# Optimization experiments

Hardware: AMD Instinct MI355X
Metric: run time of the kernel (lower is better)

The kernel has to match this reference:

```python
import jax, jax.numpy as jnp
import numpy as np

N, LQ, C, M, L, P = 8, 2048, 256, 8, 4, 4
DH = C // M  # 32
LENS = (2048, 1024, 512, 256)


def setup_inputs() -> dict:
    key = jax.random.key(0)
    ks = jax.random.split(key, 8)
    s = 1.0 / np.sqrt(C)
    return {
        "query": jax.random.normal(ks[0], (N, LQ, C), jnp.float32),
        "reference_points": jax.random.uniform(ks[1], (N, LQ, L, 1), jnp.float32),
        "input_flatten": jax.random.normal(ks[2], (N, sum(LENS), C), jnp.float32),
        "temporal_lens": np.array(LENS, np.int64),
        "level_start_index": np.array([0, 2048, 3072, 3584], np.int64),
        "W_off": jax.random.normal(ks[3], (C, M * L * P), jnp.float32) * 0.01,
        "b_off": jax.random.normal(ks[4], (M * L * P,), jnp.float32),
        "W_attn": jax.random.normal(ks[5], (C, M * L * P), jnp.float32) * 0.01,
        "b_attn": jnp.zeros((M * L * P,), jnp.float32),
        "W_val": jax.random.normal(ks[6], (C, C), jnp.float32) * s,
        "b_val": jnp.zeros((C,), jnp.float32),
        "W_out": jax.random.normal(ks[7], (C, C), jnp.float32) * s,
        "b_out": jnp.zeros((C,), jnp.float32),
    }


def _deform_core(value, lens, loc, attn):
    # value: (N, S, M, DH); loc, attn: (N, LQ, M, L, P); loc in normalized [0,1] coords.
    # Equivalent to per-level F.grid_sample (bilinear, zeros padding, align_corners=False)
    # on a 1xT image: pixel position = loc*T - 0.5; the y-coord 0.5 lands exactly on row 0.
    outs = []
    start = 0
    for l, T in enumerate(lens):
        v = value[:, start:start + T].transpose(0, 2, 1, 3)  # (N, M, T, DH)
        start += T
        pos = loc[..., l, :] * T - 0.5                       # (N, LQ, M, P)
        x0f = jnp.floor(pos)
        frac = pos - x0f
        x0 = x0f.astype(jnp.int32)

        def gather(idx):
            i = jnp.clip(idx, 0, T - 1).transpose(0, 2, 1, 3).reshape(N, M, LQ * P, 1)
            return jnp.take_along_axis(v, i, axis=2).reshape(N, M, LQ, P, DH)

        in0 = ((x0 >= 0) & (x0 < T)).astype(value.dtype)
        in1 = ((x0 + 1 >= 0) & (x0 + 1 < T)).astype(value.dtype)
        w0 = ((1.0 - frac) * in0).transpose(0, 2, 1, 3)[..., None]  # (N, M, LQ, P, 1)
        w1 = (frac * in1).transpose(0, 2, 1, 3)[..., None]
        outs.append(gather(x0) * w0 + gather(x0 + 1) * w1)          # (N, M, LQ, P, DH)
    sampled = jnp.stack(outs, axis=3)          # (N, M, LQ, L, P, DH)
    aw = attn.transpose(0, 2, 1, 3, 4)         # (N, M, LQ, L, P)
    return jnp.einsum('nmqlpd,nmqlp->nqmd', sampled, aw).reshape(N, LQ, C)


def reference(query, reference_points, input_flatten, temporal_lens, level_start_index,
              W_off, b_off, W_attn, b_attn, W_val, b_val, W_out, b_out):
    lens = [int(t) for t in np.asarray(temporal_lens)[:L]]  # static per-level lengths
    value = (input_flatten @ W_val + b_val).reshape(N, -1, M, DH)
    off = (query @ W_off + b_off).reshape(N, LQ, M, L, P)
    attn = jax.nn.softmax((query @ W_attn + b_attn).reshape(N, LQ, M, L * P), axis=-1)
    attn = attn.reshape(N, LQ, M, L, P)
    norm = jnp.asarray(lens, query.dtype)                    # offset_normalizer (L,)
    loc = reference_points[:, :, None, :, None, 0] + off / norm[None, None, None, :, None]
    out = _deform_core(value, lens, loc, attn)
    out = out @ W_out + b_out
    return out, loc, attn
```

## Files before the change

### kernel.cpp

```cpp
#include <hip/hip_runtime.h>
#include <hip/hip_bf16.h>
#include <math.h>

#define NB 8
#define LQ 2048
#define CCH 256
#define MH 8
#define SSUM 3840

typedef unsigned short ushort_t;
typedef unsigned int uint_t;
typedef __attribute__((ext_vector_type(8))) short bf16x8;
typedef __attribute__((ext_vector_type(4))) float f32x4;

__device__ inline ushort_t f2bf(float f) {
  __hip_bfloat16 h = __float2bfloat16(f);
  return *reinterpret_cast<ushort_t*>(&h);
}
__device__ inline float bf2f_lo(uint_t u) {
  union { uint_t u32; float f; } x;
  x.u32 = u << 16;
  return x.f;
}
__device__ inline float bf2f_hi(uint_t u) {
  union { uint_t u32; float f; } x;
  x.u32 = u & 0xffff0000u;
  return x.f;
}

__global__ __launch_bounds__(256) void prep_all(
    const float* __restrict__ Wv, const float* __restrict__ Wo,
    const float* __restrict__ Woff, const float* __restrict__ Wattn,
    ushort_t* __restrict__ BtVal, ushort_t* __restrict__ BtOut,
    ushort_t* __restrict__ BtOA) {
  int b = blockIdx.x;
  int k = threadIdx.x;
  if (b < 256) {
    BtVal[b * 256 + k] = f2bf(Wv[(size_t)k * 256 + b]);
  } else if (b < 512) {
    int n = b - 256;
    BtOut[n * 256 + k] = f2bf(Wo[(size_t)k * 256 + n]);
  } else if (b < 640) {
    int n = b - 512;
    BtOA[n * 256 + k] = f2bf(Woff[(size_t)k * 128 + n]);
  } else {
    int n = b - 640;
    BtOA[(128 + n) * 256 + k] = f2bf(Wattn[(size_t)k * 128 + n]);
  }
}

template <typename AT, typename OT>
__global__ __launch_bounds__(256) void gemm_mfma(
    const AT* __restrict__ A, const ushort_t* __restrict__ Bt,
    const float* __restrict__ bias0, const float* __restrict__ bias1,
    OT* __restrict__ C0, OT* __restrict__ C1,
    int Nsplit, int Cstride) {
  __shared__ ushort_t Abf[2][128][24];
  __shared__ ushort_t Bbf[2][128][24];

  const int tid = threadIdx.x;
  const int bm = blockIdx.y * 128;
  const int bn = blockIdx.x * 128;

  const int lane = tid & 63;
  const int wv = tid >> 6;
  const int wm = (wv >> 1) * 64;
  const int wn = (wv & 1) * 64;
  const int quad = lane >> 4;
  const int l16 = lane & 15;

  const int sr = tid & 127;
  const int sh = tid >> 7;

  f32x4 acc[4][4];
#pragma unroll
  for (int i = 0; i < 4; ++i)
#pragma unroll
    for (int j = 0; j < 4; ++j) acc[i][j] = (f32x4)(0.f);

  for (int k0 = 0; k0 < 256; k0 += 32) {
    uint4 aq0, aq1;
    if constexpr (sizeof(AT) == 4) {
      const float* gp = (const float*)A + (size_t)(bm + sr) * 256 + k0 + sh * 16;
      float4 f0 = *(const float4*)(gp + 0);
      float4 f1 = *(const float4*)(gp + 4);
      float4 f2 = *(const float4*)(gp + 8);
      float4 f3 = *(const float4*)(gp + 12);
      aq0.x = (uint_t)f2bf(f0.x) | ((uint_t)f2bf(f0.y) << 16);
      aq0.y = (uint_t)f2bf(f0.z) | ((uint_t)f2bf(f0.w) << 16);
      aq0.z = (uint_t)f2bf(f1.x) | ((uint_t)f2bf(f1.y) << 16);
      aq0.w = (uint_t)f2bf(f1.z) | ((uint_t)f2bf(f1.w) << 16);
      aq1.x = (uint_t)f2bf(f2.x) | ((uint_t)f2bf(f2.y) << 16);
      aq1.y = (uint_t)f2bf(f2.z) | ((uint_t)f2bf(f2.w) << 16);
      aq1.z = (uint_t)f2bf(f3.x) | ((uint_t)f2bf(f3.y) << 16);
      aq1.w = (uint_t)f2bf(f3.z) | ((uint_t)f2bf(f3.w) << 16);
    } else {
      const ushort_t* gp = (const ushort_t*)A + (size_t)(bm + sr) * 256 + k0 + sh * 16;
      aq0 = *(const uint4*)(gp + 0);
      aq1 = *(const uint4*)(gp + 8);
    }
    const ushort_t* gb = Bt + (size_t)(bn + sr) * 256 + k0 + sh * 16;
    uint4 bq0 = *(const uint4*)(gb + 0);
    uint4 bq1 = *(const uint4*)(gb + 8);

    __syncthreads();
    *(uint4*)&Abf[sh][sr][0] = aq0;
    *(uint4*)&Abf[sh][sr][8] = aq1;
    *(uint4*)&Bbf[sh][sr][0] = bq0;
    *(uint4*)&Bbf[sh][sr][8] = bq1;
    __syncthreads();

    bf16x8 af[4], bfr[4];
#pragma unroll
    for (int mi = 0; mi < 4; ++mi)
      af[mi] = *(const bf16x8*)&Abf[quad >> 1][wm + mi * 16 + l16][(quad & 1) * 8];
#pragma unroll
    for (int ni = 0; ni < 4; ++ni)
      bfr[ni] = *(const bf16x8*)&Bbf[quad >> 1][wn + ni * 16 + l16][(quad & 1) * 8];
#pragma unroll
    for (int mi = 0; mi < 4; ++mi)
#pragma unroll
      for (int ni = 0; ni < 4; ++ni)
        acc[mi][ni] = __builtin_amdgcn_mfma_f32_16x16x32_bf16(af[mi], bfr[ni], acc[mi][ni], 0, 0, 0);
  }

  const int cbase = (bn < Nsplit) ? bn : bn - Nsplit;
  OT* C = (bn < Nsplit) ? C0 : C1;
  const float* bias = (bn < Nsplit) ? bias0 : bias1;

#pragma unroll
  for (int ni = 0; ni < 4; ++ni) {
    int cc = cbase + wn + ni * 16 + l16;
    float bv = bias[cc];
#pragma unroll
    for (int mi = 0; mi < 4; ++mi) {
      f32x4 v = acc[mi][ni];
      int rbase = bm + wm + mi * 16 + ((lane >> 4) << 2);
#pragma unroll
      for (int r = 0; r < 4; ++r) {
        float o = v[r] + bv;
        if constexpr (sizeof(OT) == 4)
          C[(size_t)(rbase + r) * Cstride + cc] = o;
        else
          C[(size_t)(rbase + r) * Cstride + cc] = f2bf(o);
      }
    }
  }
}

__global__ __launch_bounds__(256) void deform_fused(
    const ushort_t* __restrict__ value,
    float* __restrict__ locbuf,
    float* __restrict__ attnbuf,
    const float* __restrict__ refp,
    ushort_t* __restrict__ core) {
  const int tid = threadIdx.x;
  const int nq0 = blockIdx.x * 4;
  const int n = nq0 >> 11;

  __shared__ float slv[512];
  __shared__ float slog[512];
  __shared__ float4 sp[512];

  const float rnorm[4] = {1.f / 2048.f, 1.f / 1024.f, 1.f / 512.f, 1.f / 256.f};
  const int lensA[4] = {2048, 1024, 512, 256};
  const int startsA[4] = {0, 2048, 3072, 3584};

#pragma unroll
  for (int j = 0; j < 2; ++j) {
    int s = tid + j * 256;
    int q = s >> 7;
    int r = s & 127;
    int l = (r >> 2) & 3;
    float lv = refp[(size_t)(nq0 + q) * 4 + l] +
               locbuf[(size_t)nq0 * 128 + s] * rnorm[l];
    locbuf[(size_t)nq0 * 128 + s] = lv;
    slv[s] = lv;
    slog[s] = attnbuf[(size_t)nq0 * 128 + s];
  }
  __syncthreads();

  if (tid < 32) {
    int base = tid * 16;
    float v[16];
#pragma unroll
    for (int i = 0; i < 16; ++i) v[i] = slog[base + i];
    float mx = v[0];
#pragma unroll
    for (int i = 1; i < 16; ++i) mx = fmaxf(mx, v[i]);
    float ssum = 0.f;
#pragma unroll
    for (int i = 0; i < 16; ++i) { v[i] = __expf(v[i] - mx); ssum += v[i]; }
    float rs = 1.f / ssum;
    float* gout = attnbuf + (size_t)nq0 * 128 + base;
#pragma unroll
    for (int i = 0; i < 16; ++i) {
      float pv = v[i] * rs;
      slog[base + i] = pv;
      gout[i] = pv;
    }
  }
  __syncthreads();

#pragma unroll
  for (int j = 0; j < 2; ++j) {
    int s = tid + j * 256;
    int q = s >> 7;
    int r = s & 127;
    int m = r >> 4;
    int lp = r & 15;
    int l = lp >> 2;
    int T = lensA[l];
    float lv = slv[s];
    float aw = slog[s];
    float pos = lv * (float)T - 0.5f;
    float x0f = floorf(pos);
    float fr = pos - x0f;
    int x0 = (int)x0f;
    float w0 = ((unsigned)x0 < (unsigned)T) ? (1.f - fr) * aw : 0.f;
    float w1 = ((unsigned)(x0 + 1) < (unsigned)T) ? fr * aw : 0.f;
    int i0 = min(max(x0, 0), T - 1);
    int i1 = min(max(x0 + 1, 0), T - 1);
    float4 pr;
    pr.x = w0;
    pr.y = w1;
    pr.z = __int_as_float((startsA[l] + i0) * 256);
    pr.w = __int_as_float((startsA[l] + i1) * 256);
    sp[q * 128 + lp * 8 + m] = pr;
  }
  __syncthreads();

  const int q = tid >> 6;
  const int t64 = tid & 63;
  const int m = t64 >> 3;
  const int g = t64 & 7;
  const ushort_t* vbase = value + (size_t)n * (SSUM * 256) + m * 32 + g * 4;

  float a0 = 0.f, a1 = 0.f, a2 = 0.f, a3 = 0.f;
#pragma unroll
  for (int lp = 0; lp < 16; ++lp) {
    float4 pr = sp[q * 128 + lp * 8 + m];
    int o0 = __float_as_int(pr.z);
    int o1 = __float_as_int(pr.w);
    uint2 u0 = *(const uint2*)(vbase + o0);
    uint2 u1 = *(const uint2*)(vbase + o1);
    a0 += pr.x * bf2f_lo(u0.x) + pr.y * bf2f_lo(u1.x);
    a1 += pr.x * bf2f_hi(u0.x) + pr.y * bf2f_hi(u1.x);
    a2 += pr.x * bf2f_lo(u0.y) + pr.y * bf2f_lo(u1.y);
    a3 += pr.x * bf2f_hi(u0.y) + pr.y * bf2f_hi(u1.y);
  }
  uint2 outp;
  outp.x = (uint_t)f2bf(a0) | ((uint_t)f2bf(a1) << 16);
  outp.y = (uint_t)f2bf(a2) | ((uint_t)f2bf(a3) << 16);
  *(uint2*)&core[(size_t)(nq0 + q) * 256 + m * 32 + g * 4] = outp;
}

extern "C" void kernel_launch(void* const* d_in, const int* in_sizes, int n_in,
                              void* d_out, int out_size, void* d_ws, size_t ws_size,
                              hipStream_t stream) {
  const float* query    = (const float*)d_in[0];
  const float* refpts   = (const float*)d_in[1];
  const float* in_flat  = (const float*)d_in[2];
  const float* W_off  = (const float*)d_in[5];
  const float* b_off  = (const float*)d_in[6];
  const float* W_attn = (const float*)d_in[7];
  const float* b_attn = (const float*)d_in[8];
  const float* W_val  = (const float*)d_in[9];
  const float* b_val  = (const float*)d_in[10];
  const float* W_out  = (const float*)d_in[11];
  const float* b_out  = (const float*)d_in[12];

  float* out  = (float*)d_out;
  float* loc  = out + (size_t)NB * LQ * CCH;
  float* attn = loc + (size_t)NB * LQ * 128;

  ushort_t* value = (ushort_t*)d_ws;
  ushort_t* core  = value + (size_t)NB * SSUM * CCH;
  ushort_t* BtVal = core + (size_t)NB * LQ * CCH;
  ushort_t* BtOut = BtVal + 256 * 256;
  ushort_t* BtOA  = BtOut + 256 * 256;

  const int Mq = NB * LQ;
  const int Mv = NB * SSUM;

  prep_all<<<768, 256, 0, stream>>>(W_val, W_out, W_off, W_attn, BtVal, BtOut, BtOA);

  gemm_mfma<float, ushort_t><<<dim3(2, Mv / 128), 256, 0, stream>>>(
      in_flat, BtVal, b_val, b_val, value, value, 1 << 30, 256);

  gemm_mfma<float, float><<<dim3(2, Mq / 128), 256, 0, stream>>>(
      query, BtOA, b_off, b_attn, loc, attn, 128, 128);

  deform_fused<<<Mq / 4, 256, 0, stream>>>(value, loc, attn, refpts, core);

  gemm_mfma<ushort_t, float><<<dim3(2, Mq / 128), 256, 0, stream>>>(
      core, BtOut, b_out, b_out, out, out, 1 << 30, 256);
}
```

Baseline: 179.0 us.

## Retile GEMMs to 64x256 blocks and stage epilogue through LDS for vector stores

The GEMM kernel now gives each block a 64-row by full-256-column tile, so every A row is read and converted from fp32 once instead of twice across two column blocks. The accumulator layout changes to 2x8 MFMA tiles per wave. The epilogue writes results into a shared-memory buffer (unioned with the operand tiles) and then emits coalesced float4 or packed bf16 stores instead of scattered scalar stores. In exchange, the whole 256-row B tile is loaded into LDS on every k step, only half the threads load A, and more barriers are needed.

```diff
diff --git a/kernel.cpp b/kernel.cpp
--- a/kernel.cpp
+++ b/kernel.cpp
@@ -55,94 +55,127 @@
     const float* __restrict__ bias0, const float* __restrict__ bias1,
     OT* __restrict__ C0, OT* __restrict__ C1,
     int Nsplit, int Cstride) {
-  __shared__ ushort_t Abf[2][128][24];
-  __shared__ ushort_t Bbf[2][128][24];
+  __shared__ union {
+    struct {
+      ushort_t Abf[2][64][24];
+      ushort_t Bbf[2][256][24];
+    } s;
+    float sout[4][16][132];
+  } u;
 
   const int tid = threadIdx.x;
-  const int bm = blockIdx.y * 128;
-  const int bn = blockIdx.x * 128;
+  const int bm = blockIdx.y * 64;
 
   const int lane = tid & 63;
   const int wv = tid >> 6;
-  const int wm = (wv >> 1) * 64;
-  const int wn = (wv & 1) * 64;
+  const int wm = (wv >> 1) * 32;
+  const int wn = (wv & 1) * 128;
   const int quad = lane >> 4;
   const int l16 = lane & 15;
 
-  const int sr = tid & 127;
-  const int sh = tid >> 7;
-
-  f32x4 acc[4][4];
-#pragma unroll
-  for (int i = 0; i < 4; ++i)
-#pragma unroll
-    for (int j = 0; j < 4; ++j) acc[i][j] = (f32x4)(0.f);
+  float bv[8];
+#pragma unroll
+  for (int ni = 0; ni < 8; ++ni) {
+    int c = wn + ni * 16 + l16;
+    bv[ni] = (c < Nsplit) ? bias0[c] : bias1[c - Nsplit];
+  }
+
+  f32x4 acc[2][8];
+#pragma unroll
+  for (int i = 0; i < 2; ++i)
+#pragma unroll
+    for (int j = 0; j < 8; ++j) acc[i][j] = (f32x4)(0.f);
+
+  const int arow = tid >> 1, ahalf = tid & 1;
 
   for (int k0 = 0; k0 < 256; k0 += 32) {
-    uint4 aq0, aq1;
-    if constexpr (sizeof(AT) == 4) {
-      const float* gp = (const float*)A + (size_t)(bm + sr) * 256 + k0 + sh * 16;
-      float4 f0 = *(const float4*)(gp + 0);
-      float4 f1 = *(const float4*)(gp + 4);
-      float4 f2 = *(const float4*)(gp + 8);
-      float4 f3 = *(const float4*)(gp + 12);
-      aq0.x = (uint_t)f2bf(f0.x) | ((uint_t)f2bf(f0.y) << 16);
-      aq0.y = (uint_t)f2bf(f0.z) | ((uint_t)f2bf(f0.w) << 16);
-      aq0.z = (uint_t)f2bf(f1.x) | ((uint_t)f2bf(f1.y) << 16);
-      aq0.w = (uint_t)f2bf(f1.z) | ((uint_t)f2bf(f1.w) << 16);
-      aq1.x = (uint_t)f2bf(f2.x) | ((uint_t)f2bf(f2.y) << 16);
-      aq1.y = (uint_t)f2bf(f2.z) | ((uint_t)f2bf(f2.w) << 16);
-      aq1.z = (uint_t)f2bf(f3.x) | ((uint_t)f2bf(f3.y) << 16);
-      aq1.w = (uint_t)f2bf(f3.z) | ((uint_t)f2bf(f3.w) << 16);
+    uint4 aq;
+    if (tid < 128) {
+      if constexpr (sizeof(AT) == 4) {
+        const float* gp = (const float*)A + (size_t)(bm + arow) * 256 + k0 + ahalf * 16;
+        float4 f0 = *(const float4*)(gp + 0);
+        float4 f1 = *(const float4*)(gp + 4);
+        float4 f2 = *(const float4*)(gp + 8);
+        float4 f3 = *(const float4*)(gp + 12);
+        aq.x = (uint_t)f2bf(f0.x) | ((uint_t)f2bf(f0.y) << 16);
+        aq.y = (uint_t)f2bf(f0.z) | ((uint_t)f2bf(f0.w) << 16);
+        aq.z = (uint_t)f2bf(f1.x) | ((uint_t)f2bf(f1.y) << 16);
+        aq.w = (uint_t)f2bf(f1.z) | ((uint_t)f2bf(f1.w) << 16);
+        uint4 aq2;
+        aq2.x = (uint_t)f2bf(f2.x) | ((uint_t)f2bf(f2.y) << 16);
+        aq2.y = (uint_t)f2bf(f2.z) | ((uint_t)f2bf(f2.w) << 16);
+        aq2.z = (uint_t)f2bf(f3.x) | ((uint_t)f2bf(f3.y) << 16);
+        aq2.w = (uint_t)f2bf(f3.z) | ((uint_t)f2bf(f3.w) << 16);
+        __syncthreads();
+        *(uint4*)&u.s.Abf[ahalf][arow][0] = aq;
+        *(uint4*)&u.s.Abf[ahalf][arow][8] = aq2;
+      } else {
+        const ushort_t* gp = (const ushort_t*)A + (size_t)(bm + arow) * 256 + k0 + ahalf * 16;
+        aq = *(const uint4*)(gp + 0);
+        uint4 aq2 = *(const uint4*)(gp + 8);
+        __syncthreads();
+        *(uint4*)&u.s.Abf[ahalf][arow][0] = aq;
+        *(uint4*)&u.s.Abf[ahalf][arow][8] = aq2;
+      }
     } else {
-      const ushort_t* gp = (const ushort_t*)A + (size_t)(bm + sr) * 256 + k0 + sh * 16;
-      aq0 = *(const uint4*)(gp + 0);
-      aq1 = *(const uint4*)(gp + 8);
-    }
-    const ushort_t* gb = Bt + (size_t)(bn + sr) * 256 + k0 + sh * 16;
-    uint4 bq0 = *(const uint4*)(gb + 0);
-    uint4 bq1 = *(const uint4*)(gb + 8);
-
+      __syncthreads();
+    }
+    {
+      const ushort_t* gb = Bt + (size_t)tid * 256 + k0;
+      uint4 b0 = *(const uint4*)(gb + 0);
+      uint4 b1 = *(const uint4*)(gb + 8);
+      uint4 b2 = *(const uint4*)(gb + 16);
+      uint4 b3 = *(const uint4*)(gb + 24);
+      *(uint4*)&u.s.Bbf[0][tid][0] = b0;
+      *(uint4*)&u.s.Bbf[0][tid][8] = b1;
+      *(uint4*)&u.s.Bbf[1][tid][0] = b2;
+      *(uint4*)&u.s.Bbf[1][tid][8] = b3;
+    }
     __syncthreads();
-    *(uint4*)&Abf[sh][sr][0] = aq0;
-    *(uint4*)&Abf[sh][sr][8] = aq1;
-    *(uint4*)&Bbf[sh][sr][0] = bq0;
-    *(uint4*)&Bbf[sh][sr][8] = bq1;
+
+    bf16x8 af[2], bfr[8];
+#pragma unroll
+    for (int mi = 0; mi < 2; ++mi)
+      af[mi] = *(const bf16x8*)&u.s.Abf[quad >> 1][wm + mi * 16 + l16][(quad & 1) * 8];
+#pragma unroll
+    for (int ni = 0; ni < 8; ++ni)
+      bfr[ni] = *(const bf16x8*)&u.s.Bbf[quad >> 1][wn + ni * 16 + l16][(quad & 1) * 8];
+#pragma unroll
+    for (int mi = 0; mi < 2; ++mi)
+#pragma unroll
+      for (int ni = 0; ni < 8; ++ni)
+        acc[mi][ni] = __builtin_amdgcn_mfma_f32_16x16x32_bf16(af[mi], bfr[ni], acc[mi][ni], 0, 0, 0);
+  }
+
+  const int l32 = lane & 31;
+  const int rhi = lane >> 5;
+#pragma unroll
+  for (int mi = 0; mi < 2; ++mi) {
     __syncthreads();
-
-    bf16x8 af[4], bfr[4];
-#pragma unroll
-    for (int mi = 0; mi < 4; ++mi)
-      af[mi] = *(const bf16x8*)&Abf[quad >> 1][wm + mi * 16 + l16][(quad & 1) * 8];
-#pragma unroll
-    for (int ni = 0; ni < 4; ++ni)
-      bfr[ni] = *(const bf16x8*)&Bbf[quad >> 1][wn + ni * 16 + l16][(quad & 1) * 8];
-#pragma unroll
-    for (int mi = 0; mi < 4; ++mi)
-#pragma unroll
-      for (int ni = 0; ni < 4; ++ni)
-        acc[mi][ni] = __builtin_amdgcn_mfma_f32_16x16x32_bf16(af[mi], bfr[ni], acc[mi][ni], 0, 0, 0);
-  }
-
-  const int cbase = (bn < Nsplit) ? bn : bn - Nsplit;
-  OT* C = (bn < Nsplit) ? C0 : C1;
-  const float* bias = (bn < Nsplit) ? bias0 : bias1;
-
-#pragma unroll
-  for (int ni = 0; ni < 4; ++ni) {
-    int cc = cbase + wn + ni * 16 + l16;
-    float bv = bias[cc];
-#pragma unroll
-    for (int mi = 0; mi < 4; ++mi) {
+#pragma unroll
+    for (int ni = 0; ni < 8; ++ni) {
       f32x4 v = acc[mi][ni];
-      int rbase = bm + wm + mi * 16 + ((lane >> 4) << 2);
-#pragma unroll
-      for (int r = 0; r < 4; ++r) {
-        float o = v[r] + bv;
-        if constexpr (sizeof(OT) == 4)
-          C[(size_t)(rbase + r) * Cstride + cc] = o;
-        else
-          C[(size_t)(rbase + r) * Cstride + cc] = f2bf(o);
+#pragma unroll
+      for (int r = 0; r < 4; ++r)
+        u.sout[wv][quad * 4 + r][ni * 16 + l16] = v[r] + bv[ni];
+    }
+    __syncthreads();
+#pragma unroll
+    for (int j = 0; j < 8; ++j) {
+      int lrow = j * 2 + rhi;
+      float4 v = *(const float4*)&u.sout[wv][lrow][l32 * 4];
+      int grow = bm + wm + mi * 16 + lrow;
+      int gcol = wn + l32 * 4;
+      int cc; OT* C;
+      if (gcol < Nsplit) { C = C0; cc = gcol; }
+      else { C = C1; cc = gcol - Nsplit; }
+      if constexpr (sizeof(OT) == 4) {
+        *(float4*)&((float*)C)[(size_t)grow * Cstride + cc] = v;
+      } else {
+        uint2 o;
+        o.x = (uint_t)f2bf(v.x) | ((uint_t)f2bf(v.y) << 16);
+        o.y = (uint_t)f2bf(v.z) | ((uint_t)f2bf(v.w) << 16);
+        *(uint2*)&((ushort_t*)C)[(size_t)grow * Cstride + cc] = o;
       }
     }
   }
@@ -285,14 +318,14 @@
 
   prep_all<<<768, 256, 0, stream>>>(W_val, W_out, W_off, W_attn, BtVal, BtOut, BtOA);
 
-  gemm_mfma<float, ushort_t><<<dim3(2, Mv / 128), 256, 0, stream>>>(
+  gemm_mfma<float, ushort_t><<<dim3(1, Mv / 64), 256, 0, stream>>>(
       in_flat, BtVal, b_val, b_val, value, value, 1 << 30, 256);
 
-  gemm_mfma<float, float><<<dim3(2, Mq / 128), 256, 0, stream>>>(
+  gemm_mfma<float, float><<<dim3(1, Mq / 64), 256, 0, stream>>>(
       query, BtOA, b_off, b_attn, loc, attn, 128, 128);
 
   deform_fused<<<Mq / 4, 256, 0, stream>>>(value, loc, attn, refpts, core);
 
-  gemm_mfma<ushort_t, float><<<dim3(2, Mq / 128), 256, 0, stream>>>(
+  gemm_mfma<ushort_t, float><<<dim3(1, Mq / 64), 256, 0, stream>>>(
       core, BtOut, b_out, b_out, out, out, 1 << 30, 256);
 }
```

Measured after the change: 187.9 us. 1.05x slower.

## Fuse weight conversion into GEMMs and merge value/offset GEMMs into one launch

Applied to the files above, without the earlier changes.

Removes the separate weight transpose/bf16-conversion kernel. Each GEMM block now reads fp32 weights directly, converts them to bf16 and scatters them transposed into shared memory. The value projection and the offset/attention projection are merged into a single multi-job launch, and the output projection reuses the same kernel with a job offset. The float-to-bf16 packing also switches to a paired conversion intrinsic. This saves two launches and the prep pass, but it adds strided fp32 weight loads and scalar shared-memory scatter stores inside every k-step, plus runtime branching on pointer types.

```diff
diff --git a/kernel.cpp b/kernel.cpp
--- a/kernel.cpp
+++ b/kernel.cpp
@@ -5,7 +5,6 @@
 #define NB 8
 #define LQ 2048
 #define CCH 256
-#define MH 8
 #define SSUM 3840
 
 typedef unsigned short ushort_t;
@@ -17,6 +16,11 @@
   __hip_bfloat16 h = __float2bfloat16(f);
   return *reinterpret_cast<ushort_t*>(&h);
 }
+__device__ inline uint_t pk2bf(float lo, float hi) {
+  float2 t; t.x = lo; t.y = hi;
+  __hip_bfloat162 h = __float22bfloat162_rn(t);
+  return *reinterpret_cast<uint_t*>(&h);
+}
 __device__ inline float bf2f_lo(uint_t u) {
   union { uint_t u32; float f; } x;
   x.u32 = u << 16;
@@ -28,49 +32,54 @@
   return x.f;
 }
 
-__global__ __launch_bounds__(256) void prep_all(
-    const float* __restrict__ Wv, const float* __restrict__ Wo,
-    const float* __restrict__ Woff, const float* __restrict__ Wattn,
-    ushort_t* __restrict__ BtVal, ushort_t* __restrict__ BtOut,
-    ushort_t* __restrict__ BtOA) {
-  int b = blockIdx.x;
-  int k = threadIdx.x;
-  if (b < 256) {
-    BtVal[b * 256 + k] = f2bf(Wv[(size_t)k * 256 + b]);
-  } else if (b < 512) {
-    int n = b - 256;
-    BtOut[n * 256 + k] = f2bf(Wo[(size_t)k * 256 + n]);
-  } else if (b < 640) {
-    int n = b - 512;
-    BtOA[n * 256 + k] = f2bf(Woff[(size_t)k * 128 + n]);
-  } else {
-    int n = b - 640;
-    BtOA[(128 + n) * 256 + k] = f2bf(Wattn[(size_t)k * 128 + n]);
-  }
-}
-
-template <typename AT, typename OT>
-__global__ __launch_bounds__(256) void gemm_mfma(
-    const AT* __restrict__ A, const ushort_t* __restrict__ Bt,
-    const float* __restrict__ bias0, const float* __restrict__ bias1,
-    OT* __restrict__ C0, OT* __restrict__ C1,
-    int Nsplit, int Cstride) {
+__global__ __launch_bounds__(256) void gemm_multi(
+    int job_base,
+    const float* __restrict__ in_flat, const float* __restrict__ query,
+    const ushort_t* __restrict__ core,
+    const float* __restrict__ W_val, const float* __restrict__ W_off,
+    const float* __restrict__ W_attn, const float* __restrict__ W_out,
+    const float* __restrict__ b_val, const float* __restrict__ b_off,
+    const float* __restrict__ b_attn, const float* __restrict__ b_out,
+    ushort_t* __restrict__ value, float* __restrict__ loc,
+    float* __restrict__ attn, float* __restrict__ out) {
   __shared__ ushort_t Abf[2][128][24];
   __shared__ ushort_t Bbf[2][128][24];
 
+  const int job = job_base + blockIdx.x;
+
+  const float* Af = nullptr;
+  const ushort_t* Ab16 = nullptr;
+  const float* W; const float* bias;
+  int wstride, wcol, bm, cstride, colbase;
+  float* Cf = nullptr; ushort_t* Cb = nullptr;
+
+  if (job < 480) {
+    int bn = (job & 1) * 128; bm = (job >> 1) * 128;
+    Af = in_flat; W = W_val; wstride = 256; wcol = bn;
+    bias = b_val + bn; Cb = value; cstride = 256; colbase = bn;
+  } else if (job < 736) {
+    int p = job - 480; bm = (p >> 1) * 128;
+    Af = query;
+    if (p & 1) { W = W_attn; bias = b_attn; Cf = attn; }
+    else       { W = W_off;  bias = b_off;  Cf = loc;  }
+    wstride = 128; wcol = 0; cstride = 128; colbase = 0;
+  } else {
+    int o = job - 736; int bn = (o & 1) * 128; bm = (o >> 1) * 128;
+    Ab16 = core; W = W_out; wstride = 256; wcol = bn;
+    bias = b_out + bn; Cf = out; cstride = 256; colbase = bn;
+  }
+
   const int tid = threadIdx.x;
-  const int bm = blockIdx.y * 128;
-  const int bn = blockIdx.x * 128;
-
   const int lane = tid & 63;
   const int wv = tid >> 6;
   const int wm = (wv >> 1) * 64;
   const int wn = (wv & 1) * 64;
   const int quad = lane >> 4;
   const int l16 = lane & 15;
-
   const int sr = tid & 127;
   const int sh = tid >> 7;
+  const int kq = tid >> 5;
+  const int ln = tid & 31;
 
   f32x4 acc[4][4];
 #pragma unroll
@@ -80,34 +89,39 @@
 
   for (int k0 = 0; k0 < 256; k0 += 32) {
     uint4 aq0, aq1;
-    if constexpr (sizeof(AT) == 4) {
-      const float* gp = (const float*)A + (size_t)(bm + sr) * 256 + k0 + sh * 16;
+    if (Af) {
+      const float* gp = Af + (size_t)(bm + sr) * 256 + k0 + sh * 16;
       float4 f0 = *(const float4*)(gp + 0);
       float4 f1 = *(const float4*)(gp + 4);
       float4 f2 = *(const float4*)(gp + 8);
       float4 f3 = *(const float4*)(gp + 12);
-      aq0.x = (uint_t)f2bf(f0.x) | ((uint_t)f2bf(f0.y) << 16);
-      aq0.y = (uint_t)f2bf(f0.z) | ((uint_t)f2bf(f0.w) << 16);
-      aq0.z = (uint_t)f2bf(f1.x) | ((uint_t)f2bf(f1.y) << 16);
-      aq0.w = (uint_t)f2bf(f1.z) | ((uint_t)f2bf(f1.w) << 16);
-      aq1.x = (uint_t)f2bf(f2.x) | ((uint_t)f2bf(f2.y) << 16);
-      aq1.y = (uint_t)f2bf(f2.z) | ((uint_t)f2bf(f2.w) << 16);
-      aq1.z = (uint_t)f2bf(f3.x) | ((uint_t)f2bf(f3.y) << 16);
-      aq1.w = (uint_t)f2bf(f3.z) | ((uint_t)f2bf(f3.w) << 16);
+      aq0.x = pk2bf(f0.x, f0.y); aq0.y = pk2bf(f0.z, f0.w);
+      aq0.z = pk2bf(f1.x, f1.y); aq0.w = pk2bf(f1.z, f1.w);
+      aq1.x = pk2bf(f2.x, f2.y); aq1.y = pk2bf(f2.z, f2.w);
+      aq1.z = pk2bf(f3.x, f3.y); aq1.w = pk2bf(f3.z, f3.w);
     } else {
-      const ushort_t* gp = (const ushort_t*)A + (size_t)(bm + sr) * 256 + k0 + sh * 16;
+      const ushort_t* gp = Ab16 + (size_t)(bm + sr) * 256 + k0 + sh * 16;
       aq0 = *(const uint4*)(gp + 0);
       aq1 = *(const uint4*)(gp + 8);
     }
-    const ushort_t* gb = Bt + (size_t)(bn + sr) * 256 + k0 + sh * 16;
-    uint4 bq0 = *(const uint4*)(gb + 0);
-    uint4 bq1 = *(const uint4*)(gb + 8);
+    float wreg[16];
+#pragma unroll
+    for (int j = 0; j < 4; ++j) {
+      const float* wp = W + (size_t)(k0 + kq + j * 8) * wstride + wcol + ln;
+#pragma unroll
+      for (int nb = 0; nb < 4; ++nb) wreg[j * 4 + nb] = wp[nb * 32];
+    }
 
     __syncthreads();
     *(uint4*)&Abf[sh][sr][0] = aq0;
     *(uint4*)&Abf[sh][sr][8] = aq1;
-    *(uint4*)&Bbf[sh][sr][0] = bq0;
-    *(uint4*)&Bbf[sh][sr][8] = bq1;
+#pragma unroll
+    for (int j = 0; j < 4; ++j) {
+      int k = kq + j * 8;
+#pragma unroll
+      for (int nb = 0; nb < 4; ++nb)
+        Bbf[k >> 4][ln + nb * 32][k & 15] = f2bf(wreg[j * 4 + nb]);
+    }
     __syncthreads();
 
     bf16x8 af[4], bfr[4];
@@ -124,25 +138,20 @@
         acc[mi][ni] = __builtin_amdgcn_mfma_f32_16x16x32_bf16(af[mi], bfr[ni], acc[mi][ni], 0, 0, 0);
   }
 
-  const int cbase = (bn < Nsplit) ? bn : bn - Nsplit;
-  OT* C = (bn < Nsplit) ? C0 : C1;
-  const float* bias = (bn < Nsplit) ? bias0 : bias1;
-
 #pragma unroll
   for (int ni = 0; ni < 4; ++ni) {
-    int cc = cbase + wn + ni * 16 + l16;
+    int cc = wn + ni * 16 + l16;
     float bv = bias[cc];
 #pragma unroll
     for (int mi = 0; mi < 4; ++mi) {
       f32x4 v = acc[mi][ni];
-      int rbase = bm + wm + mi * 16 + ((lane >> 4) << 2);
+      int rbase = bm + wm + mi * 16 + quad * 4;
 #pragma unroll
       for (int r = 0; r < 4; ++r) {
         float o = v[r] + bv;
-        if constexpr (sizeof(OT) == 4)
-          C[(size_t)(rbase + r) * Cstride + cc] = o;
-        else
-          C[(size_t)(rbase + r) * Cstride + cc] = f2bf(o);
+        size_t idx = (size_t)(rbase + r) * cstride + colbase + cc;
+        if (Cb) Cb[idx] = f2bf(o);
+        else    Cf[idx] = o;
       }
     }
   }
@@ -276,23 +285,16 @@
 
   ushort_t* value = (ushort_t*)d_ws;
   ushort_t* core  = value + (size_t)NB * SSUM * CCH;
-  ushort_t* BtVal = core + (size_t)NB * LQ * CCH;
-  ushort_t* BtOut = BtVal + 256 * 256;
-  ushort_t* BtOA  = BtOut + 256 * 256;
 
   const int Mq = NB * LQ;
-  const int Mv = NB * SSUM;
-
-  prep_all<<<768, 256, 0, stream>>>(W_val, W_out, W_off, W_attn, BtVal, BtOut, BtOA);
-
-  gemm_mfma<float, ushort_t><<<dim3(2, Mv / 128), 256, 0, stream>>>(
-      in_flat, BtVal, b_val, b_val, value, value, 1 << 30, 256);
-
-  gemm_mfma<float, float><<<dim3(2, Mq / 128), 256, 0, stream>>>(
-      query, BtOA, b_off, b_attn, loc, attn, 128, 128);
+
+  gemm_multi<<<736, 256, 0, stream>>>(
+      0, in_flat, query, core, W_val, W_off, W_attn, W_out,
+      b_val, b_off, b_attn, b_out, value, loc, attn, out);
 
   deform_fused<<<Mq / 4, 256, 0, stream>>>(value, loc, attn, refpts, core);
 
-  gemm_mfma<ushort_t, float><<<dim3(2, Mq / 128), 256, 0, stream>>>(
-      core, BtOut, b_out, b_out, out, out, 1 << 30, 256);
-}
+  gemm_multi<<<256, 256, 0, stream>>>(
+      736, in_flat, query, core, W_val, W_off, W_attn, W_out,
+      b_val, b_off, b_attn, b_out, value, loc, attn, out);
+}
```

After: 180.9 us. No clear change (+1.0%).
